# Performance work log

Hardware: AMD Instinct MI355X
Metric: run time of the kernel (lower is better)

The kernel has to match this reference:

```python
import jax, jax.numpy as jnp
import numpy as np

ORDER = 256     # N (HiPPO order)
A_DIAG = -0.5   # LagT: A = -(tril(ones) + a*I), a = -0.5
B_COEF = 1.0    # B = b * ones, b = 1


def toeplitz_mult(a, x):
    """Lower-triangular Toeplitz matvec = causal truncated convolution along last axis.
    a: (..., N) first column of the Toeplitz operator; x: (..., N)."""
    N = a.shape[-1]
    F = 2 * N
    af = jnp.fft.rfft(a, n=F, axis=-1)
    xf = jnp.fft.rfft(x, n=F, axis=-1)
    return jnp.fft.irfft(af * xf, n=F, axis=-1)[..., :N]


def forward_mult(u, delta):
    # (I + delta*A) u with A = -(tril(ones) + a*I):  u - delta*(cumsum(u) + a*u)
    return u - delta[..., None] * (jnp.cumsum(u, axis=-1) + A_DIAG * u)


def inverse_mult(u, delta):
    # (I - delta*A)^{-1} u. I - delta*A = c*I + delta*StrictLowerOnes, c = 1 + delta*(1+a).
    # Its inverse is lower-tri Toeplitz with first column [1/c, -(r/c), -(r/c)(1-r), ...], r = delta/c.
    N = u.shape[-1]
    d = delta[..., None]
    c = 1.0 + d * (1.0 + A_DIAG)
    r = d / c
    tail = -(r / c) * (1.0 - r) ** jnp.arange(N - 1, dtype=u.dtype)  # (..., N-1)
    kernel = jnp.concatenate([1.0 / c, tail], axis=-1)               # (..., N)
    return toeplitz_mult(kernel, u)


def bilinear(dt, u, v, alpha=0.5):
    # (I - alpha*dt*A)^{-1} [ (I + (1-alpha)*dt*A) u + dt * B * v ]
    x = forward_mult(u, (1.0 - alpha) * dt)
    x = x + (dt * v)[..., None] * B_COEF
    return inverse_mult(x, alpha * dt)


def setup_inputs() -> dict:
    key = jax.random.key(0)
    k1, k2 = jax.random.split(key)
    L, B, M = 1024, 4, 64
    inputs = jax.random.normal(k1, (L, B, M), dtype=jnp.float32)
    dt = jax.random.uniform(k2, (L, B, M), dtype=jnp.float32)
    return {"inputs": inputs, "dt": dt}


def reference(inputs, dt):
    L, B, M = inputs.shape
    N = ORDER
    e = jnp.zeros((N,), inputs.dtype).at[0].set(1.0)
    I = jnp.broadcast_to(e, (L, B, M, N))
    As = bilinear(dt, I, jnp.zeros_like(dt))       # (L,B,M,N) first columns of transition Toeplitz ops
    Bs = bilinear(dt, jnp.zeros_like(I), inputs)   # (L,B,M,N) discretized input contributions

    def step(x, ab):
        a, b = ab
        x = toeplitz_mult(a, x) + b                # x_l = A_l x_{l-1} + B_l  (variable_unroll_toeplitz)
        return x, x

    _, out = jax.lax.scan(step, jnp.zeros((B, M, N), inputs.dtype), (As, Bs))
    return out  # (L, B, M, N)
```

## Files before the change

kernel.cpp:

```cpp
#include <hip/hip_runtime.h>


namespace {

constexpr int LLEN   = 1024;
constexpr int NCHAN  = 256;
constexpr int KCH    = 32;
constexpr int SKEW   = 96;
constexpr int RSLOT  = 128;
constexpr int NCHUNK = 43;
constexpr int GPAD   = 1152;

constexpr int G_OFF = 0;
constexpr int B_OFF = GPAD;
constexpr int R_OFF = 2 * GPAD;
constexpr int LDS_FLOATS = R_OFF + 4 * RSLOT * 64;
constexpr size_t LDS_BYTES = (size_t)LDS_FLOATS * 4;

using f32x4 = __attribute__((ext_vector_type(4))) float;

__device__ __forceinline__ float dpp_shr1(float v) {
    return __int_as_float(__builtin_amdgcn_update_dpp(
        0, __float_as_int(v), 0x138 , 0xF, 0xF, false));
}

__device__ __forceinline__ void compiler_mem_fence() {
    asm volatile("" ::: "memory");
}

__device__ __forceinline__ void lds_barrier() {
    __builtin_amdgcn_sched_barrier(0);
    asm volatile("s_waitcnt lgkmcnt(0)" ::: "memory");
    __builtin_amdgcn_s_barrier();
    __builtin_amdgcn_sched_barrier(0);
}

template <bool W0, bool MASKED>
__device__ __forceinline__ void do_chunk(
    const int T0, const int bl, const int lane, const bool lane0,
    const float* __restrict__ g_arr, const float* __restrict__ hb_src,
    float* __restrict__ my_ring, float& prev_own, float& prev_left)
{
    float hb[KCH];
    if (W0) {
        #pragma unroll
        for (int q = 0; q < KCH / 4; ++q) {
            const f32x4 t =
                *reinterpret_cast<const f32x4*>(hb_src + T0 + 4 * q);
            hb[4*q+0] = t[0]; hb[4*q+1] = t[1];
            hb[4*q+2] = t[2]; hb[4*q+3] = t[3];
        }
    } else {
        #pragma unroll
        for (int s = 0; s < KCH; ++s)
            hb[s] = hb_src[(((bl + s) & (RSLOT - 1)) << 6) + 63];
    }

    const int m0 = bl - lane;
    #pragma unroll
    for (int s = 0; s < KCH; ++s) {
        int li = m0 + s;
        if (MASKED) li = min(max(li, 0), LLEN - 1);
        const float gg = g_arr[li];
        float cl = dpp_shr1(prev_own);
        float ct;
        if (W0) {
            ct = (lane0 ? hb[s] : 0.0f) - prev_left;
        } else {
            cl += lane0 ? hb[s] : 0.0f;
            ct = 0.0f - prev_left;
        }
        const float x = fmaf(gg, cl, fmaf(gg, prev_own, ct));
        my_ring[(((m0 + s) & (RSLOT - 1)) << 6) + lane] = x;
        if (MASKED) {
            const bool act = (unsigned)(m0 + s) < (unsigned)LLEN;
            prev_left = act ? cl : prev_left;
            prev_own  = act ? x  : prev_own;
        } else {
            prev_left = cl;
            prev_own  = x;
        }
    }
}

__global__ __launch_bounds__(256, 1)
void toeplitz_scan(const float* __restrict__ vin,
                   const float* __restrict__ dtin,
                   float* __restrict__ out)
{
    extern __shared__ float lds[];
    float* g_arr = lds + G_OFF;
    float* b_arr = lds + B_OFF;
    float* ring  = lds + R_OFF;

    const int ch  = blockIdx.x;
    const int tid = threadIdx.x;

    #pragma unroll
    for (int k = 0; k < LLEN / 256; ++k) {
        const int l = tid + 256 * k;
        const float d = dtin[l * NCHAN + ch];
        const float u = vin[l * NCHAN + ch];
        const float ic = 1.0f / (1.0f + 0.25f * d);
        g_arr[l] = (1.0f - 0.25f * d) * ic;
        b_arr[l] = d * u * ic;
    }
    if (tid < GPAD - LLEN) {
        g_arr[LLEN + tid] = 1.0f;
        b_arr[LLEN + tid] = 0.0f;
    }
    __syncthreads();

    const int wave = tid >> 6, lane = tid & 63;
    const bool w0    = (wave == 0);
    const bool lane0 = (lane == 0);
    const int wskew  = wave * SKEW;

    float* my_ring = ring + wave * (RSLOT * 64);
    const float* lf_ring = ring + (wave - 1) * (RSLOT * 64);

    float prev_own = 0.0f, prev_left = 0.0f;

    const int rq = lane >> 4;
    const int cq = (lane & 15) << 2;
    float* const out_col = out + (size_t)(ch * 256 + wave * 64 + cq);

    for (int c = 0; c < NCHUNK; ++c) {
        const int T0 = c * KCH;
        const int bl = T0 - wskew;

        if (bl >= 0 && bl <= 1056) {
            const bool fast = (bl >= 64) && (bl <= LLEN - KCH);
            if (w0) {
                if (fast)
                    do_chunk<true, false>(T0, bl, lane, lane0, g_arr, b_arr,
                                          my_ring, prev_own, prev_left);
                else
                    do_chunk<true, true>(T0, bl, lane, lane0, g_arr, b_arr,
                                         my_ring, prev_own, prev_left);
            } else {
                if (fast)
                    do_chunk<false, false>(T0, bl, lane, lane0, g_arr, lf_ring,
                                           my_ring, prev_own, prev_left);
                else
                    do_chunk<false, true>(T0, bl, lane, lane0, g_arr, lf_ring,
                                          my_ring, prev_own, prev_left);
            }
        }

        const int F = T0 - wskew - 64;
        if (F >= 0 && F <= LLEN - KCH) {
            compiler_mem_fence();
            const float* rb = my_ring + ((F & (RSLOT - 1)) << 6) + cq;
            float* ob = out_col + (size_t)(F + rq) * (NCHAN * 256);
            #pragma unroll
            for (int q = 0; q < 8; ++q) {
                const f32x4 v =
                    *reinterpret_cast<const f32x4*>(rb + ((4 * q + rq) << 6));
                __builtin_nontemporal_store(v, reinterpret_cast<f32x4*>(ob));
                ob += (size_t)4 * (NCHAN * 256);
            }
        }
        lds_barrier();
    }
}

}

extern "C" void kernel_launch(void* const* d_in, const int* in_sizes, int n_in,
                              void* d_out, int out_size, void* d_ws, size_t ws_size,
                              hipStream_t stream) {
    (void)in_sizes; (void)n_in; (void)d_ws; (void)ws_size; (void)out_size;
    const float* vin  = (const float*)d_in[0];
    const float* dtin = (const float*)d_in[1];
    float* out = (float*)d_out;

    (void)hipFuncSetAttribute(reinterpret_cast<const void*>(toeplitz_scan),
                              hipFuncAttributeMaxDynamicSharedMemorySize,
                              (int)LDS_BYTES);

    toeplitz_scan<<<NCHAN, 256, LDS_BYTES, stream>>>(vin, dtin, out);
}
```

Before: 65.63 us.

## Batch LDS loads with inline asm and overlap output flush with chunk compute

Rewrites the per-chunk body so that all LDS reads (ring data for output flush, g coefficients, halo values) are issued up front as inline-asm ds_read instructions behind a single lgkmcnt wait, then the recurrence runs from registers. The flush of a previous chunk is delayed by one more chunk (F = bl-96, one extra iteration) and merged into the same body, so its global stores overlap with the recurrence. This aims to hide LDS latency and store issue behind compute, at the cost of more registers and an extra loop iteration.

```diff
diff --git a/kernel.cpp b/kernel.cpp
--- a/kernel.cpp
+++ b/kernel.cpp
@@ -8,7 +8,7 @@
 constexpr int KCH    = 32;
 constexpr int SKEW   = 96;
 constexpr int RSLOT  = 128;
-constexpr int NCHUNK = 43;
+constexpr int NCHUNK = 44;
 constexpr int GPAD   = 1152;
 
 constexpr int G_OFF = 0;
@@ -23,11 +23,22 @@
     return __int_as_float(__builtin_amdgcn_update_dpp(
         0, __float_as_int(v), 0x138 , 0xF, 0xF, false));
 }
-
-__device__ __forceinline__ void compiler_mem_fence() {
-    asm volatile("" ::: "memory");
-}
-
+__device__ __forceinline__ unsigned lds_a(const void* p) {
+    return (unsigned)(unsigned long long)p;
+}
+__device__ __forceinline__ void ds_rd32(float& d, unsigned a, int imm) {
+    asm volatile("ds_read_b32 %0, %1 offset:%2" : "=v"(d) : "v"(a), "i"(imm));
+}
+__device__ __forceinline__ void ds_rd128(f32x4& d, unsigned a, int imm) {
+    asm volatile("ds_read_b128 %0, %1 offset:%2" : "=v"(d) : "v"(a), "i"(imm));
+}
+__device__ __forceinline__ void ds_wr32(unsigned a, float x) {
+    asm volatile("ds_write_b32 %0, %1" :: "v"(a), "v"(x));
+}
+__device__ __forceinline__ void wait_lgkm0_fence() {
+    asm volatile("s_waitcnt lgkmcnt(0)" ::: "memory");
+    __builtin_amdgcn_sched_barrier(0);
+}
 __device__ __forceinline__ void lds_barrier() {
     __builtin_amdgcn_sched_barrier(0);
     asm volatile("s_waitcnt lgkmcnt(0)" ::: "memory");
@@ -35,50 +46,94 @@
     __builtin_amdgcn_sched_barrier(0);
 }
 
-template <bool W0, bool MASKED>
-__device__ __forceinline__ void do_chunk(
-    const int T0, const int bl, const int lane, const bool lane0,
-    const float* __restrict__ g_arr, const float* __restrict__ hb_src,
-    float* __restrict__ my_ring, float& prev_own, float& prev_left)
+template <bool W0, int TMODE>
+__device__ __forceinline__ void chunk_body(
+    const int T0, const int bl, const bool doF, const int lane,
+    const unsigned g_base, const unsigned b_base,
+    const unsigned lf_base, const unsigned my_base,
+    float& prev_own, float& prev_left,
+    float* __restrict__ out_fl)
 {
-    float hb[KCH];
-    if (W0) {
-        #pragma unroll
-        for (int q = 0; q < KCH / 4; ++q) {
-            const f32x4 t =
-                *reinterpret_cast<const f32x4*>(hb_src + T0 + 4 * q);
-            hb[4*q+0] = t[0]; hb[4*q+1] = t[1];
-            hb[4*q+2] = t[2]; hb[4*q+3] = t[3];
-        }
-    } else {
-        #pragma unroll
-        for (int s = 0; s < KCH; ++s)
-            hb[s] = hb_src[(((bl + s) & (RSLOT - 1)) << 6) + 63];
-    }
-
-    const int m0 = bl - lane;
-    #pragma unroll
-    for (int s = 0; s < KCH; ++s) {
-        int li = m0 + s;
-        if (MASKED) li = min(max(li, 0), LLEN - 1);
-        const float gg = g_arr[li];
-        float cl = dpp_shr1(prev_own);
-        float ct;
+    const int F = bl - 96;
+    f32x4 tmp4[8];
+    float gpre[KCH], hb[KCH];
+
+    if (doF) {
+        const unsigned fb = my_base +
+            (unsigned)((((F & (RSLOT - 1)) + (lane >> 4)) << 8) + ((lane & 15) << 4));
+        #pragma unroll
+        for (int q = 0; q < 8; ++q) ds_rd128(tmp4[q], fb, q * 1024);
+    }
+    if (TMODE == 2) {
+        const unsigned ga = g_base + 4u * (unsigned)(bl - lane);
+        #pragma unroll
+        for (int s = 0; s < KCH; ++s) ds_rd32(gpre[s], ga, 4 * s);
+    } else if (TMODE == 1) {
+        #pragma unroll
+        for (int s = 0; s < KCH; ++s) {
+            const int li = min(max(bl - lane + s, 0), LLEN - 1);
+            ds_rd32(gpre[s], g_base + 4u * (unsigned)li, 0);
+        }
+    }
+    if (TMODE > 0) {
         if (W0) {
-            ct = (lane0 ? hb[s] : 0.0f) - prev_left;
+            const unsigned ba = b_base + 4u * (unsigned)T0;
+            #pragma unroll
+            for (int q = 0; q < KCH / 4; ++q) {
+                f32x4 t; ds_rd128(t, ba, 16 * q);
+                hb[4*q+0] = t[0]; hb[4*q+1] = t[1];
+                hb[4*q+2] = t[2]; hb[4*q+3] = t[3];
+            }
         } else {
-            cl += lane0 ? hb[s] : 0.0f;
-            ct = 0.0f - prev_left;
-        }
-        const float x = fmaf(gg, cl, fmaf(gg, prev_own, ct));
-        my_ring[(((m0 + s) & (RSLOT - 1)) << 6) + lane] = x;
-        if (MASKED) {
-            const bool act = (unsigned)(m0 + s) < (unsigned)LLEN;
-            prev_left = act ? cl : prev_left;
-            prev_own  = act ? x  : prev_own;
-        } else {
-            prev_left = cl;
-            prev_own  = x;
+            const unsigned ha = lf_base + (unsigned)(((bl & (RSLOT - 1)) << 8) + 252);
+            #pragma unroll
+            for (int s = 0; s < KCH; ++s) ds_rd32(hb[s], ha, s << 8);
+        }
+    }
+    wait_lgkm0_fence();
+
+    if (TMODE > 0) {
+        const bool lane0 = (lane == 0);
+        float hbm[KCH];
+        #pragma unroll
+        for (int s = 0; s < KCH; ++s) hbm[s] = lane0 ? hb[s] : 0.0f;
+
+        unsigned soff = (unsigned)((((bl - lane) & (RSLOT - 1)) << 8));
+        const unsigned colb = my_base + ((unsigned)lane << 2);
+        #pragma unroll
+        for (int s = 0; s < KCH; ++s) {
+            const float u = dpp_shr1(prev_own);
+            const float gg = gpre[s];
+            float x, npl;
+            if (W0) {
+                const float t1 = fmaf(gg, prev_own, hbm[s] - prev_left);
+                x = fmaf(gg, u, t1);
+                npl = u;
+            } else {
+                const float ua = u + hbm[s];
+                const float t1 = fmaf(gg, prev_own, -prev_left);
+                x = fmaf(gg, ua, t1);
+                npl = ua;
+            }
+            ds_wr32(colb + soff, x);
+            soff = (soff + 256u) & 32767u;
+            if (TMODE == 1) {
+                const bool act = (unsigned)(bl - lane + s) < (unsigned)LLEN;
+                prev_left = act ? npl : prev_left;
+                prev_own  = act ? x   : prev_own;
+            } else {
+                prev_left = npl;
+                prev_own  = x;
+            }
+        }
+    }
+
+    if (doF) {
+        float* ob = out_fl + (size_t)(F + (lane >> 4)) * (NCHAN * 256);
+        #pragma unroll
+        for (int q = 0; q < 8; ++q) {
+            __builtin_nontemporal_store(tmp4[q], reinterpret_cast<f32x4*>(ob));
+            ob += (size_t)4 * (NCHAN * 256);
         }
     }
 }
@@ -112,54 +167,40 @@
     __syncthreads();
 
     const int wave = tid >> 6, lane = tid & 63;
-    const bool w0    = (wave == 0);
-    const bool lane0 = (lane == 0);
-    const int wskew  = wave * SKEW;
-
-    float* my_ring = ring + wave * (RSLOT * 64);
-    const float* lf_ring = ring + (wave - 1) * (RSLOT * 64);
+    const bool w0   = (wave == 0);
+    const int wskew = wave * SKEW;
+
+    const unsigned g_base  = lds_a(g_arr);
+    const unsigned b_base  = lds_a(b_arr);
+    const unsigned my_base = lds_a(ring + wave * (RSLOT * 64));
+    const unsigned lf_base = lds_a(ring + (wave - 1) * (RSLOT * 64));
 
     float prev_own = 0.0f, prev_left = 0.0f;
-
-    const int rq = lane >> 4;
-    const int cq = (lane & 15) << 2;
-    float* const out_col = out + (size_t)(ch * 256 + wave * 64 + cq);
+    float* const out_fl = out + (size_t)(ch * 256 + wave * 64 + (lane & 15) * 4);
 
     for (int c = 0; c < NCHUNK; ++c) {
         const int T0 = c * KCH;
         const int bl = T0 - wskew;
-
-        if (bl >= 0 && bl <= 1056) {
-            const bool fast = (bl >= 64) && (bl <= LLEN - KCH);
-            if (w0) {
-                if (fast)
-                    do_chunk<true, false>(T0, bl, lane, lane0, g_arr, b_arr,
-                                          my_ring, prev_own, prev_left);
-                else
-                    do_chunk<true, true>(T0, bl, lane, lane0, g_arr, b_arr,
-                                         my_ring, prev_own, prev_left);
+        const int F  = bl - 96;
+        const bool doF   = (F >= 0) && (F <= LLEN - KCH);
+        const bool ticks = (bl >= 0) && (bl <= 1056);
+        const bool fast  = (bl >= 64) && (bl <= LLEN - KCH);
+
+        if (ticks) {
+            if (fast) {
+                if (w0) chunk_body<true, 2>(T0, bl, doF, lane, g_base, b_base,
+                                            lf_base, my_base, prev_own, prev_left, out_fl);
+                else    chunk_body<false, 2>(T0, bl, doF, lane, g_base, b_base,
+                                             lf_base, my_base, prev_own, prev_left, out_fl);
             } else {
-                if (fast)
-                    do_chunk<false, false>(T0, bl, lane, lane0, g_arr, lf_ring,
-                                           my_ring, prev_own, prev_left);
-                else
-                    do_chunk<false, true>(T0, bl, lane, lane0, g_arr, lf_ring,
-                                          my_ring, prev_own, prev_left);
-            }
-        }
-
-        const int F = T0 - wskew - 64;
-        if (F >= 0 && F <= LLEN - KCH) {
-            compiler_mem_fence();
-            const float* rb = my_ring + ((F & (RSLOT - 1)) << 6) + cq;
-            float* ob = out_col + (size_t)(F + rq) * (NCHAN * 256);
-            #pragma unroll
-            for (int q = 0; q < 8; ++q) {
-                const f32x4 v =
-                    *reinterpret_cast<const f32x4*>(rb + ((4 * q + rq) << 6));
-                __builtin_nontemporal_store(v, reinterpret_cast<f32x4*>(ob));
-                ob += (size_t)4 * (NCHAN * 256);
-            }
+                if (w0) chunk_body<true, 1>(T0, bl, doF, lane, g_base, b_base,
+                                            lf_base, my_base, prev_own, prev_left, out_fl);
+                else    chunk_body<false, 1>(T0, bl, doF, lane, g_base, b_base,
+                                             lf_base, my_base, prev_own, prev_left, out_fl);
+            }
+        } else if (doF) {
+            chunk_body<false, 0>(T0, bl, true, lane, g_base, b_base,
+                                 lf_base, my_base, prev_own, prev_left, out_fl);
         }
         lds_barrier();
     }
```

After: 68.31 us. 1.04x slower.

## Split compute and store roles into separate producer/consumer waves

Applied to the files above, without the earlier changes.

Doubles the block to 512 threads. Four waves run the recurrence scan and write into LDS rings, and four new waves copy finished ring slots to global memory, lagging one chunk behind, with one chunk added to drain them. The goal is to take the global store traffic off the critical-path compute waves so stores overlap the sequential scan. In exchange each chunk barrier now spans twice as many waves, and ring reuse safety depends on the chosen lag.

```diff
diff --git a/kernel.cpp b/kernel.cpp
--- a/kernel.cpp
+++ b/kernel.cpp
@@ -8,7 +8,7 @@
 constexpr int KCH    = 32;
 constexpr int SKEW   = 96;
 constexpr int RSLOT  = 128;
-constexpr int NCHUNK = 43;
+constexpr int NCHUNK = 44;
 constexpr int GPAD   = 1152;
 
 constexpr int G_OFF = 0;
@@ -22,10 +22,6 @@
 __device__ __forceinline__ float dpp_shr1(float v) {
     return __int_as_float(__builtin_amdgcn_update_dpp(
         0, __float_as_int(v), 0x138 , 0xF, 0xF, false));
-}
-
-__device__ __forceinline__ void compiler_mem_fence() {
-    asm volatile("" ::: "memory");
 }
 
 __device__ __forceinline__ void lds_barrier() {
@@ -83,7 +79,7 @@
     }
 }
 
-__global__ __launch_bounds__(256, 1)
+__global__ __launch_bounds__(512, 1)
 void toeplitz_scan(const float* __restrict__ vin,
                    const float* __restrict__ dtin,
                    float* __restrict__ out)
@@ -97,8 +93,8 @@
     const int tid = threadIdx.x;
 
     #pragma unroll
-    for (int k = 0; k < LLEN / 256; ++k) {
-        const int l = tid + 256 * k;
+    for (int k = 0; k < LLEN / 512; ++k) {
+        const int l = tid + 512 * k;
         const float d = dtin[l * NCHAN + ch];
         const float u = vin[l * NCHAN + ch];
         const float ic = 1.0f / (1.0f + 0.25f * d);
@@ -111,57 +107,66 @@
     }
     __syncthreads();
 
-    const int wave = tid >> 6, lane = tid & 63;
-    const bool w0    = (wave == 0);
-    const bool lane0 = (lane == 0);
-    const int wskew  = wave * SKEW;
+    const int wv = tid >> 6, lane = tid & 63;
 
-    float* my_ring = ring + wave * (RSLOT * 64);
-    const float* lf_ring = ring + (wave - 1) * (RSLOT * 64);
+    if (wv < 4) {
+        const int w = wv;
+        const bool w0    = (w == 0);
+        const bool lane0 = (lane == 0);
+        const int wskew  = w * SKEW;
+        float* my_ring = ring + w * (RSLOT * 64);
+        const float* lf_ring = ring + (w > 0 ? (w - 1) : 0) * (RSLOT * 64);
+        float prev_own = 0.0f, prev_left = 0.0f;
 
-    float prev_own = 0.0f, prev_left = 0.0f;
+        for (int c = 0; c < NCHUNK; ++c) {
+            const int T0 = c * KCH;
+            const int bl = T0 - wskew;
+            if (bl >= 0 && bl <= 1056) {
+                const bool fast = (bl >= 64) && (bl <= LLEN - KCH);
+                if (w0) {
+                    if (fast)
+                        do_chunk<true, false>(T0, bl, lane, lane0, g_arr,
+                                              b_arr, my_ring, prev_own, prev_left);
+                    else
+                        do_chunk<true, true>(T0, bl, lane, lane0, g_arr,
+                                             b_arr, my_ring, prev_own, prev_left);
+                } else {
+                    if (fast)
+                        do_chunk<false, false>(T0, bl, lane, lane0, g_arr,
+                                               lf_ring, my_ring, prev_own, prev_left);
+                    else
+                        do_chunk<false, true>(T0, bl, lane, lane0, g_arr,
+                                              lf_ring, my_ring, prev_own, prev_left);
+                }
+            }
+            lds_barrier();
+        }
+    } else {
+        const int sw = wv - 4;
+        const float* sring = ring + sw * (RSLOT * 64);
+        const int rq = lane >> 4;
+        const int cq = (lane & 15) << 2;
+        float* const out_fl =
+            out + (size_t)(ch * 256 + sw * 64 + cq);
+        const int lag = sw * SKEW + 96;
 
-    const int rq = lane >> 4;
-    const int cq = (lane & 15) << 2;
-    float* const out_col = out + (size_t)(ch * 256 + wave * 64 + cq);
-
-    for (int c = 0; c < NCHUNK; ++c) {
-        const int T0 = c * KCH;
-        const int bl = T0 - wskew;
-
-        if (bl >= 0 && bl <= 1056) {
-            const bool fast = (bl >= 64) && (bl <= LLEN - KCH);
-            if (w0) {
-                if (fast)
-                    do_chunk<true, false>(T0, bl, lane, lane0, g_arr, b_arr,
-                                          my_ring, prev_own, prev_left);
-                else
-                    do_chunk<true, true>(T0, bl, lane, lane0, g_arr, b_arr,
-                                         my_ring, prev_own, prev_left);
-            } else {
-                if (fast)
-                    do_chunk<false, false>(T0, bl, lane, lane0, g_arr, lf_ring,
-                                           my_ring, prev_own, prev_left);
-                else
-                    do_chunk<false, true>(T0, bl, lane, lane0, g_arr, lf_ring,
-                                          my_ring, prev_own, prev_left);
+        for (int c = 0; c < NCHUNK; ++c) {
+            const int F = c * KCH - lag;
+            if (F >= 0 && F <= LLEN - KCH) {
+                const float* rb = sring + ((F & (RSLOT - 1)) << 6) + cq;
+                f32x4 v[8];
+                #pragma unroll
+                for (int q = 0; q < 8; ++q)
+                    v[q] = *reinterpret_cast<const f32x4*>(rb + ((4*q + rq) << 6));
+                float* ob = out_fl + (size_t)(F + rq) * (NCHAN * 256);
+                #pragma unroll
+                for (int q = 0; q < 8; ++q) {
+                    __builtin_nontemporal_store(v[q], reinterpret_cast<f32x4*>(ob));
+                    ob += (size_t)4 * (NCHAN * 256);
+                }
             }
+            lds_barrier();
         }
-
-        const int F = T0 - wskew - 64;
-        if (F >= 0 && F <= LLEN - KCH) {
-            compiler_mem_fence();
-            const float* rb = my_ring + ((F & (RSLOT - 1)) << 6) + cq;
-            float* ob = out_col + (size_t)(F + rq) * (NCHAN * 256);
-            #pragma unroll
-            for (int q = 0; q < 8; ++q) {
-                const f32x4 v =
-                    *reinterpret_cast<const f32x4*>(rb + ((4 * q + rq) << 6));
-                __builtin_nontemporal_store(v, reinterpret_cast<f32x4*>(ob));
-                ob += (size_t)4 * (NCHAN * 256);
-            }
-        }
-        lds_barrier();
     }
 }
 
@@ -179,5 +184,5 @@
                               hipFuncAttributeMaxDynamicSharedMemorySize,
                               (int)LDS_BYTES);
 
-    toeplitz_scan<<<NCHAN, 256, LDS_BYTES, stream>>>(vin, dtin, out);
+    toeplitz_scan<<<NCHAN, 512, LDS_BYTES, stream>>>(vin, dtin, out);
 }
```

After: 70.77 us. 7.8% more time.

## Split compute into single producer wave with four store waves via LDS flags

Applied to the files above, without the earlier changes.

Replaces the four skewed compute waves, which synchronised with a block barrier every chunk, with one producer wave. Each lane of that wave computes four adjacent state entries per time step. Four additional consumer waves poll LDS flags and stream the ring rows to global memory with nontemporal stores. The aim is to remove the per-chunk barriers and the cross-wave diagonal skew, and to overlap output stores with the recurrence. The cost is a longer serial dependency chain in the single compute wave and spin-polling on LDS.

```diff
diff --git a/kernel.cpp b/kernel.cpp
--- a/kernel.cpp
+++ b/kernel.cpp
@@ -3,87 +3,87 @@
 
 namespace {
 
-constexpr int LLEN   = 1024;
-constexpr int NCHAN  = 256;
-constexpr int KCH    = 32;
-constexpr int SKEW   = 96;
-constexpr int RSLOT  = 128;
-constexpr int NCHUNK = 43;
-constexpr int GPAD   = 1152;
+constexpr int LLEN  = 1024;
+constexpr int NCHAN = 256;
+constexpr int KCH   = 32;
+constexpr int NCHC  = 34;
+constexpr int RROWS = 128;
+constexpr int RSTR  = 264;
+constexpr int GPAD  = 1152;
 
 constexpr int G_OFF = 0;
 constexpr int B_OFF = GPAD;
-constexpr int R_OFF = 2 * GPAD;
-constexpr int LDS_FLOATS = R_OFF + 4 * RSLOT * 64;
+constexpr int F_OFF = 2 * GPAD;
+constexpr int R_OFF = F_OFF + 8;
+constexpr int LDS_FLOATS = R_OFF + RROWS * RSTR;
 constexpr size_t LDS_BYTES = (size_t)LDS_FLOATS * 4;
 
 using f32x4 = __attribute__((ext_vector_type(4))) float;
+using i32x4 = __attribute__((ext_vector_type(4))) int;
 
 __device__ __forceinline__ float dpp_shr1(float v) {
     return __int_as_float(__builtin_amdgcn_update_dpp(
         0, __float_as_int(v), 0x138 , 0xF, 0xF, false));
 }
-
-__device__ __forceinline__ void compiler_mem_fence() {
-    asm volatile("" ::: "memory");
+__device__ __forceinline__ unsigned lds_addr(const void* p) {
+    return (unsigned)(unsigned long long)p;
+}
+__device__ __forceinline__ int poll_i32(const int* p) {
+    int v;
+    asm volatile("ds_read_b32 %0, %1\n\ts_waitcnt lgkmcnt(0)"
+                 : "=v"(v) : "v"(lds_addr(p)) : "memory");
+    return v;
+}
+__device__ __forceinline__ i32x4 poll_i32x4(const int* p) {
+    i32x4 v;
+    asm volatile("ds_read_b128 %0, %1\n\ts_waitcnt lgkmcnt(0)"
+                 : "=v"(v) : "v"(lds_addr(p)) : "memory");
+    return v;
+}
+__device__ __forceinline__ void publish_i32(int* p, int val) {
+    asm volatile("s_waitcnt lgkmcnt(0)\n\tds_write_b32 %0, %1"
+                 :: "v"(lds_addr(p)), "v"(val) : "memory");
 }
 
-__device__ __forceinline__ void lds_barrier() {
-    __builtin_amdgcn_sched_barrier(0);
-    asm volatile("s_waitcnt lgkmcnt(0)" ::: "memory");
-    __builtin_amdgcn_s_barrier();
-    __builtin_amdgcn_sched_barrier(0);
-}
-
-template <bool W0, bool MASKED>
-__device__ __forceinline__ void do_chunk(
-    const int T0, const int bl, const int lane, const bool lane0,
-    const float* __restrict__ g_arr, const float* __restrict__ hb_src,
-    float* __restrict__ my_ring, float& prev_own, float& prev_left)
+template <bool MASKED>
+__device__ __forceinline__ void ticks32(
+    const int T0, const int lane, const bool lane0,
+    const float* __restrict__ g_arr, const float* __restrict__ b_arr,
+    float* __restrict__ ring,
+    float& p0, float& p1, float& p2, float& p3, float& p3p)
 {
-    float hb[KCH];
-    if (W0) {
-        #pragma unroll
-        for (int q = 0; q < KCH / 4; ++q) {
-            const f32x4 t =
-                *reinterpret_cast<const f32x4*>(hb_src + T0 + 4 * q);
-            hb[4*q+0] = t[0]; hb[4*q+1] = t[1];
-            hb[4*q+2] = t[2]; hb[4*q+3] = t[3];
-        }
-    } else {
-        #pragma unroll
-        for (int s = 0; s < KCH; ++s)
-            hb[s] = hb_src[(((bl + s) & (RSLOT - 1)) << 6) + 63];
-    }
-
-    const int m0 = bl - lane;
+    const int l0 = T0 - lane;
+    int slot = l0 & (RROWS - 1);
+    const int colo = lane * 4;
     #pragma unroll
     for (int s = 0; s < KCH; ++s) {
-        int li = m0 + s;
-        if (MASKED) li = min(max(li, 0), LLEN - 1);
-        const float gg = g_arr[li];
-        float cl = dpp_shr1(prev_own);
-        float ct;
-        if (W0) {
-            ct = (lane0 ? hb[s] : 0.0f) - prev_left;
+        const int l = l0 + s;
+        const int li = MASKED ? max(l, 0) : l;
+        const float g  = g_arr[li];
+        const float bv = b_arr[T0 + s];
+        const float ulc = dpp_shr1(p3);
+        const float ulp = dpp_shr1(p3p);
+        const float bsel = lane0 ? bv : 0.0f;
+        const float n0 = fmaf(g, ulc + p0, bsel - ulp);
+        const float n1 = fmaf(g, n0 + p1, -p0);
+        const float n2 = fmaf(g, n1 + p2, -p1);
+        const float n3 = fmaf(g, n2 + p3, -p2);
+        f32x4 v; v[0] = n0; v[1] = n1; v[2] = n2; v[3] = n3;
+        *reinterpret_cast<f32x4*>(&ring[slot * RSTR + colo]) = v;
+        slot = (slot + 1) & (RROWS - 1);
+        if (MASKED) {
+            const bool act = (unsigned)l < (unsigned)LLEN;
+            p3p = act ? p3 : p3p;
+            p0 = act ? n0 : p0;  p1 = act ? n1 : p1;
+            p2 = act ? n2 : p2;  p3 = act ? n3 : p3;
         } else {
-            cl += lane0 ? hb[s] : 0.0f;
-            ct = 0.0f - prev_left;
-        }
-        const float x = fmaf(gg, cl, fmaf(gg, prev_own, ct));
-        my_ring[(((m0 + s) & (RSLOT - 1)) << 6) + lane] = x;
-        if (MASKED) {
-            const bool act = (unsigned)(m0 + s) < (unsigned)LLEN;
-            prev_left = act ? cl : prev_left;
-            prev_own  = act ? x  : prev_own;
-        } else {
-            prev_left = cl;
-            prev_own  = x;
+            p3p = p3;
+            p0 = n0; p1 = n1; p2 = n2; p3 = n3;
         }
     }
 }
 
-__global__ __launch_bounds__(256, 1)
+__global__ __launch_bounds__(320, 1)
 void toeplitz_scan(const float* __restrict__ vin,
                    const float* __restrict__ dtin,
                    float* __restrict__ out)
@@ -91,77 +91,80 @@
     extern __shared__ float lds[];
     float* g_arr = lds + G_OFF;
     float* b_arr = lds + B_OFF;
+    int*   flags = (int*)lds + F_OFF;
     float* ring  = lds + R_OFF;
 
     const int ch  = blockIdx.x;
     const int tid = threadIdx.x;
 
     #pragma unroll
-    for (int k = 0; k < LLEN / 256; ++k) {
-        const int l = tid + 256 * k;
-        const float d = dtin[l * NCHAN + ch];
-        const float u = vin[l * NCHAN + ch];
-        const float ic = 1.0f / (1.0f + 0.25f * d);
-        g_arr[l] = (1.0f - 0.25f * d) * ic;
-        b_arr[l] = d * u * ic;
+    for (int k = 0; k < 4; ++k) {
+        const int l = tid + 320 * k;
+        if (l < LLEN) {
+            const float d = dtin[l * NCHAN + ch];
+            const float u = vin[l * NCHAN + ch];
+            const float ic = 1.0f / (1.0f + 0.25f * d);
+            g_arr[l] = (1.0f - 0.25f * d) * ic;
+            b_arr[l] = d * u * ic;
+        } else if (l < GPAD) {
+            g_arr[l] = 1.0f;
+            b_arr[l] = 0.0f;
+        }
     }
-    if (tid < GPAD - LLEN) {
-        g_arr[LLEN + tid] = 1.0f;
-        b_arr[LLEN + tid] = 0.0f;
-    }
+    if (tid < 8) flags[tid] = 0;
     __syncthreads();
 
-    const int wave = tid >> 6, lane = tid & 63;
-    const bool w0    = (wave == 0);
-    const bool lane0 = (lane == 0);
-    const int wskew  = wave * SKEW;
+    const int wv = tid >> 6, lane = tid & 63;
 
-    float* my_ring = ring + wave * (RSLOT * 64);
-    const float* lf_ring = ring + (wave - 1) * (RSLOT * 64);
+    if (wv == 0) {
+        const bool lane0 = (lane == 0);
+        float p0 = 0.f, p1 = 0.f, p2 = 0.f, p3 = 0.f, p3p = 0.f;
 
-    float prev_own = 0.0f, prev_left = 0.0f;
+        for (int c = 0; c < NCHC; ++c) {
+            const int T0 = c * KCH;
+            const int need = T0 - 96;
+            if (need > 0) {
+                for (;;) {
+                    const i32x4 pv = poll_i32x4(flags + 4);
+                    const int m = min(min(pv[0], pv[1]), min(pv[2], pv[3]));
+                    if (m >= need) break;
+                    __builtin_amdgcn_s_sleep(2);
+                }
+            }
+            const bool fast = (T0 >= 64) && (T0 <= 992);
+            if (fast)
+                ticks32<false>(T0, lane, lane0, g_arr, b_arr, ring,
+                               p0, p1, p2, p3, p3p);
+            else
+                ticks32<true>(T0, lane, lane0, g_arr, b_arr, ring,
+                              p0, p1, p2, p3, p3p);
+            if (lane0) publish_i32(flags + 0, T0 + KCH);
+        }
+    } else {
+        const int sw = wv - 1;
+        const int rq = lane >> 4;
+        const int colbase = sw * 64 + (lane & 15) * 4;
+        float* const outb = out + (size_t)(ch * 256 + colbase);
 
-    const int rq = lane >> 4;
-    const int cq = (lane & 15) << 2;
-    float* const out_col = out + (size_t)(ch * 256 + wave * 64 + cq);
-
-    for (int c = 0; c < NCHUNK; ++c) {
-        const int T0 = c * KCH;
-        const int bl = T0 - wskew;
-
-        if (bl >= 0 && bl <= 1056) {
-            const bool fast = (bl >= 64) && (bl <= LLEN - KCH);
-            if (w0) {
-                if (fast)
-                    do_chunk<true, false>(T0, bl, lane, lane0, g_arr, b_arr,
-                                          my_ring, prev_own, prev_left);
-                else
-                    do_chunk<true, true>(T0, bl, lane, lane0, g_arr, b_arr,
-                                         my_ring, prev_own, prev_left);
-            } else {
-                if (fast)
-                    do_chunk<false, false>(T0, bl, lane, lane0, g_arr, lf_ring,
-                                           my_ring, prev_own, prev_left);
-                else
-                    do_chunk<false, true>(T0, bl, lane, lane0, g_arr, lf_ring,
-                                          my_ring, prev_own, prev_left);
+        for (int F = 0; F <= LLEN - KCH; F += KCH) {
+            while (poll_i32(flags + 0) < F + 95)
+                __builtin_amdgcn_s_sleep(2);
+            f32x4 v[8];
+            #pragma unroll
+            for (int q = 0; q < 8; ++q) {
+                const int row = F + rq + 4 * q;
+                v[q] = *reinterpret_cast<const f32x4*>(
+                    &ring[(row & (RROWS - 1)) * RSTR + colbase]);
+            }
+            asm volatile("s_waitcnt lgkmcnt(0)" ::: "memory");
+            if (lane == 0) publish_i32(flags + 4 + sw, F + KCH);
+            #pragma unroll
+            for (int q = 0; q < 8; ++q) {
+                __builtin_nontemporal_store(
+                    v[q], reinterpret_cast<f32x4*>(
+                              outb + (size_t)(F + rq + 4 * q) * (NCHAN * 256)));
             }
         }
-
-        const int F = T0 - wskew - 64;
-        if (F >= 0 && F <= LLEN - KCH) {
-            compiler_mem_fence();
-            const float* rb = my_ring + ((F & (RSLOT - 1)) << 6) + cq;
-            float* ob = out_col + (size_t)(F + rq) * (NCHAN * 256);
-            #pragma unroll
-            for (int q = 0; q < 8; ++q) {
-                const f32x4 v =
-                    *reinterpret_cast<const f32x4*>(rb + ((4 * q + rq) << 6));
-                __builtin_nontemporal_store(v, reinterpret_cast<f32x4*>(ob));
-                ob += (size_t)4 * (NCHAN * 256);
-            }
-        }
-        lds_barrier();
     }
 }
 
@@ -179,5 +182,5 @@
                               hipFuncAttributeMaxDynamicSharedMemorySize,
                               (int)LDS_BYTES);
 
-    toeplitz_scan<<<NCHAN, 256, LDS_BYTES, stream>>>(vin, dtin, out);
+    toeplitz_scan<<<NCHAN, 320, LDS_BYTES, stream>>>(vin, dtin, out);
 }
```

Result: slower. 82.02 us (+25.0%).
